# Performance work log

Measured on AMD Instinct MI355X. Metric: run time of the kernel, lower is better.

Reference implementation:

```python
import math
import jax, jax.numpy as jnp
import numpy as np

B, H, S, D = 1, 16, 4096, 64

def setup_inputs() -> dict:
    key = jax.random.key(0)
    kq, kk, kv = jax.random.split(key, 3)
    query = jax.random.normal(kq, (B, H, S, D), dtype=jnp.float32)
    k = jax.random.normal(kk, (B, H, S, D), dtype=jnp.float32)
    value = jax.random.normal(kv, (B, H, S, D), dtype=jnp.float32)
    return {"query": query, "key": k, "value": value}

def reference(query, key, value):
    # scale_factor = 1/sqrt(head_dim) (scale arg defaults to None)
    scale = 1.0 / math.sqrt(query.shape[-1])
    # bmm1: [B,H,L,S] scores; invAttnHead applies the scale inside the hpu softmax,
    # equivalent to scaling scores before a standard softmax
    scores = jnp.einsum('bhld,bhsd->bhls', query, key) * scale
    attn = jax.nn.softmax(scores, axis=-1)
    # dropout_p defaults to 0.0 -> identity; attn_bias in the original is dead code
    return jnp.einsum('bhls,bhsd->bhld', attn, value)
```

## Files before the change

kernel.cpp:

```cpp
#include <hip/hip_runtime.h>


#define SQ 4096
#define DH 64
#define KVB 64
#define VSTRIDE 72

#define QSCALE 0.1803368801111204f

typedef __attribute__((ext_vector_type(8))) short short8;
typedef __attribute__((ext_vector_type(4))) short short4v;
typedef __attribute__((ext_vector_type(4))) float f32x4;

static __device__ __forceinline__ short f2b(float f) {
  __bf16 h = (__bf16)f;
  return (short)__builtin_bit_cast(unsigned short, h);
}

static __device__ __forceinline__ float exp2_fast(float x) {
  return __builtin_amdgcn_exp2f(x);
}

#define MFMA16(a, b, c) __builtin_amdgcn_mfma_f32_16x16x32_bf16((a), (b), (c), 0, 0, 0)

__global__ __launch_bounds__(256, 2) void attn_fwd(const float* __restrict__ Q,
                                                   const float* __restrict__ K,
                                                   const float* __restrict__ V,
                                                   float* __restrict__ O) {
  __shared__ unsigned short Klds[64 * 64];
  __shared__ unsigned short Vtlds[64 * VSTRIDE];
  __shared__ unsigned short Plds[4 * 32 * 64];

  const int bid = blockIdx.x;
  const int h = (bid & 7) + 8 * (bid >> 8);
  const int qtile = (bid >> 3) & 31;
  const int tid = threadIdx.x;
  const int w = tid >> 6;
  const int lane = tid & 63;
  const int g = lane >> 4;
  const int c16 = lane & 15;

  const float* Qh = Q + h * SQ * DH;
  const float* Kh = K + h * SQ * DH;
  const float* Vh = V + h * SQ * DH;
  float* Oh = O + h * SQ * DH;

  const int qbase = qtile * 128 + w * 32;

  const f32x4 zero4 = {0.f, 0.f, 0.f, 0.f};

  short8 qb[2][2];
#pragma unroll
  for (int qt = 0; qt < 2; ++qt) {
    const float* qr = Qh + (qbase + qt * 16 + c16) * DH + 8 * g;
#pragma unroll
    for (int c = 0; c < 2; ++c) {
      float4 a = *(const float4*)(qr + 32 * c);
      float4 b = *(const float4*)(qr + 32 * c + 4);
      short8 f;
      f[0] = f2b(a.x * QSCALE); f[1] = f2b(a.y * QSCALE);
      f[2] = f2b(a.z * QSCALE); f[3] = f2b(a.w * QSCALE);
      f[4] = f2b(b.x * QSCALE); f[5] = f2b(b.y * QSCALE);
      f[6] = f2b(b.z * QSCALE); f[7] = f2b(b.w * QSCALE);
      qb[qt][c] = f;
    }
  }

  f32x4 Oacc[2][4];
#pragma unroll
  for (int qt = 0; qt < 2; ++qt)
#pragma unroll
    for (int dt = 0; dt < 4; ++dt) Oacc[qt][dt] = zero4;
  float mrun[2] = {-INFINITY, -INFINITY};
  float lrun[2] = {0.f, 0.f};

  const int sk = 4 * (tid >> 4);
  const int sd = 4 * (tid & 15);

  for (int t = 0; t < SQ / KVB; ++t) {
    const int kv0 = t * KVB;
    __syncthreads();

    {
      const float* kb = Kh + (kv0 + sk) * DH + sd;
      const float* vb = Vh + (kv0 + sk) * DH + sd;
      float4 k0 = *(const float4*)(kb + 0 * DH);
      float4 k1 = *(const float4*)(kb + 1 * DH);
      float4 k2 = *(const float4*)(kb + 2 * DH);
      float4 k3 = *(const float4*)(kb + 3 * DH);
      float4 v0 = *(const float4*)(vb + 0 * DH);
      float4 v1 = *(const float4*)(vb + 1 * DH);
      float4 v2 = *(const float4*)(vb + 2 * DH);
      float4 v3 = *(const float4*)(vb + 3 * DH);

      short4v a;
      a[0] = f2b(k0.x); a[1] = f2b(k0.y); a[2] = f2b(k0.z); a[3] = f2b(k0.w);
      *(short4v*)&Klds[(sk + 0) * 64 + (sd ^ (((sk + 0) & 7) * 8))] = a;
      a[0] = f2b(k1.x); a[1] = f2b(k1.y); a[2] = f2b(k1.z); a[3] = f2b(k1.w);
      *(short4v*)&Klds[(sk + 1) * 64 + (sd ^ (((sk + 1) & 7) * 8))] = a;
      a[0] = f2b(k2.x); a[1] = f2b(k2.y); a[2] = f2b(k2.z); a[3] = f2b(k2.w);
      *(short4v*)&Klds[(sk + 2) * 64 + (sd ^ (((sk + 2) & 7) * 8))] = a;
      a[0] = f2b(k3.x); a[1] = f2b(k3.y); a[2] = f2b(k3.z); a[3] = f2b(k3.w);
      *(short4v*)&Klds[(sk + 3) * 64 + (sd ^ (((sk + 3) & 7) * 8))] = a;

      short4v tv;
      tv[0] = f2b(v0.x); tv[1] = f2b(v1.x); tv[2] = f2b(v2.x); tv[3] = f2b(v3.x);
      *(short4v*)&Vtlds[(sd + 0) * VSTRIDE + sk] = tv;
      tv[0] = f2b(v0.y); tv[1] = f2b(v1.y); tv[2] = f2b(v2.y); tv[3] = f2b(v3.y);
      *(short4v*)&Vtlds[(sd + 1) * VSTRIDE + sk] = tv;
      tv[0] = f2b(v0.z); tv[1] = f2b(v1.z); tv[2] = f2b(v2.z); tv[3] = f2b(v3.z);
      *(short4v*)&Vtlds[(sd + 2) * VSTRIDE + sk] = tv;
      tv[0] = f2b(v0.w); tv[1] = f2b(v1.w); tv[2] = f2b(v2.w); tv[3] = f2b(v3.w);
      *(short4v*)&Vtlds[(sd + 3) * VSTRIDE + sk] = tv;
    }
    __syncthreads();

    f32x4 sA[2][4];
#pragma unroll
    for (int kt = 0; kt < 4; ++kt) {
      const int roff = (kt * 16 + c16) * 64;
      const int sw = (c16 & 7) * 8;
      short8 ka0 = *(const short8*)&Klds[roff + ((8 * g) ^ sw)];
      short8 ka1 = *(const short8*)&Klds[roff + ((8 * g + 32) ^ sw)];
      sA[0][kt] = MFMA16(ka0, qb[0][0], zero4);
      sA[0][kt] = MFMA16(ka1, qb[0][1], sA[0][kt]);
      sA[1][kt] = MFMA16(ka0, qb[1][0], zero4);
      sA[1][kt] = MFMA16(ka1, qb[1][1], sA[1][kt]);
    }

#pragma unroll
    for (int qt = 0; qt < 2; ++qt) {
      float mx = sA[qt][0][0];
#pragma unroll
      for (int kt = 0; kt < 4; ++kt)
#pragma unroll
        for (int r = 0; r < 4; ++r) mx = fmaxf(mx, sA[qt][kt][r]);
      mx = fmaxf(mx, __shfl_xor(mx, 16));
      mx = fmaxf(mx, __shfl_xor(mx, 32));
      const float mnew = fmaxf(mrun[qt], mx);
      const float fsc = exp2_fast(mrun[qt] - mnew);
      mrun[qt] = mnew;

      float psum = 0.f;
      const int prow = (w * 32 + qt * 16 + c16) * 64;
      const int psw = (c16 & 7) * 8;
#pragma unroll
      for (int kt = 0; kt < 4; ++kt) {
        float p0 = exp2_fast(sA[qt][kt][0] - mnew);
        float p1 = exp2_fast(sA[qt][kt][1] - mnew);
        float p2 = exp2_fast(sA[qt][kt][2] - mnew);
        float p3 = exp2_fast(sA[qt][kt][3] - mnew);
        psum += (p0 + p1) + (p2 + p3);
        short4v pw;
        pw[0] = f2b(p0); pw[1] = f2b(p1); pw[2] = f2b(p2); pw[3] = f2b(p3);
        *(short4v*)&Plds[prow + ((4 * g + 16 * kt) ^ psw)] = pw;
      }
      psum += __shfl_xor(psum, 16);
      psum += __shfl_xor(psum, 32);
      lrun[qt] = lrun[qt] * fsc + psum;

      const float f0 = __shfl(fsc, 4 * g + 0);
      const float f1 = __shfl(fsc, 4 * g + 1);
      const float f2 = __shfl(fsc, 4 * g + 2);
      const float f3 = __shfl(fsc, 4 * g + 3);
#pragma unroll
      for (int dt = 0; dt < 4; ++dt) {
        Oacc[qt][dt][0] *= f0;
        Oacc[qt][dt][1] *= f1;
        Oacc[qt][dt][2] *= f2;
        Oacc[qt][dt][3] *= f3;
      }
    }

#pragma unroll
    for (int c = 0; c < 2; ++c) {
      const int koff = (8 * g + 32 * c) ^ ((c16 & 7) * 8);
      short8 pa0 = *(const short8*)&Plds[(w * 32 + c16) * 64 + koff];
      short8 pa1 = *(const short8*)&Plds[(w * 32 + 16 + c16) * 64 + koff];
#pragma unroll
      for (int dt = 0; dt < 4; ++dt) {
        const int vroff = (dt * 16 + c16) * VSTRIDE + 8 * g + 32 * c;
        short4v lo = *(const short4v*)&Vtlds[vroff];
        short4v hi = *(const short4v*)&Vtlds[vroff + 4];
        short8 vbf;
        vbf[0] = lo[0]; vbf[1] = lo[1]; vbf[2] = lo[2]; vbf[3] = lo[3];
        vbf[4] = hi[0]; vbf[5] = hi[1]; vbf[6] = hi[2]; vbf[7] = hi[3];
        Oacc[0][dt] = MFMA16(pa0, vbf, Oacc[0][dt]);
        Oacc[1][dt] = MFMA16(pa1, vbf, Oacc[1][dt]);
      }
    }
  }

#pragma unroll
  for (int qt = 0; qt < 2; ++qt) {
    const float inv = 1.0f / lrun[qt];
    const float i0 = __shfl(inv, 4 * g + 0);
    const float i1 = __shfl(inv, 4 * g + 1);
    const float i2 = __shfl(inv, 4 * g + 2);
    const float i3 = __shfl(inv, 4 * g + 3);
#pragma unroll
    for (int dt = 0; dt < 4; ++dt) {
      float* op = Oh + (qbase + qt * 16 + 4 * g) * DH + dt * 16 + c16;
      op[0 * DH] = Oacc[qt][dt][0] * i0;
      op[1 * DH] = Oacc[qt][dt][1] * i1;
      op[2 * DH] = Oacc[qt][dt][2] * i2;
      op[3 * DH] = Oacc[qt][dt][3] * i3;
    }
  }
}

extern "C" void kernel_launch(void* const* d_in, const int* in_sizes, int n_in,
                              void* d_out, int out_size, void* d_ws, size_t ws_size,
                              hipStream_t stream) {
  const float* q = (const float*)d_in[0];
  const float* k = (const float*)d_in[1];
  const float* v = (const float*)d_in[2];
  float* o = (float*)d_out;
  attn_fwd<<<dim3(512), dim3(256), 0, stream>>>(q, k, v, o);
}
```

Measured before the change: 226.2 us.

## Double-buffer K/V tiles, use 8 waves of 16 rows, skip redundant rescale

Doubles the block to 512 threads so each wave owns 16 query rows instead of 32. K/V tiles are double-buffered in LDS, with the next tile's global loads issued before the current tile's compute, which removes one barrier per iteration. Output rescaling is skipped when the wave-wide max does not grow, and s_setprio raises priority around the MFMA sections. The trade-off is more LDS, more waves per block, and K/V staging spread over twice as many threads, each of which converts less data.

```diff
diff --git a/kernel.cpp b/kernel.cpp
--- a/kernel.cpp
+++ b/kernel.cpp
@@ -4,12 +4,14 @@
 #define SQ 4096
 #define DH 64
 #define KVB 64
+#define NT (SQ / KVB)
 #define VSTRIDE 72
 
 #define QSCALE 0.1803368801111204f
 
 typedef __attribute__((ext_vector_type(8))) short short8;
 typedef __attribute__((ext_vector_type(4))) short short4v;
+typedef __attribute__((ext_vector_type(2))) short short2v;
 typedef __attribute__((ext_vector_type(4))) float f32x4;
 
 static __device__ __forceinline__ short f2b(float f) {
@@ -23,13 +25,13 @@
 
 #define MFMA16(a, b, c) __builtin_amdgcn_mfma_f32_16x16x32_bf16((a), (b), (c), 0, 0, 0)
 
-__global__ __launch_bounds__(256, 2) void attn_fwd(const float* __restrict__ Q,
+__global__ __launch_bounds__(512, 4) void attn_fwd(const float* __restrict__ Q,
                                                    const float* __restrict__ K,
                                                    const float* __restrict__ V,
                                                    float* __restrict__ O) {
-  __shared__ unsigned short Klds[64 * 64];
-  __shared__ unsigned short Vtlds[64 * VSTRIDE];
-  __shared__ unsigned short Plds[4 * 32 * 64];
+  __shared__ unsigned short Klds[2][64 * 64];
+  __shared__ unsigned short Vtlds[2][64 * VSTRIDE];
+  __shared__ unsigned short Plds[8 * 16 * 64];
 
   const int bid = blockIdx.x;
   const int h = (bid & 7) + 8 * (bid >> 8);
@@ -45,14 +47,13 @@
   const float* Vh = V + h * SQ * DH;
   float* Oh = O + h * SQ * DH;
 
-  const int qbase = qtile * 128 + w * 32;
+  const int qbase = qtile * 128 + w * 16;
 
   const f32x4 zero4 = {0.f, 0.f, 0.f, 0.f};
 
-  short8 qb[2][2];
-#pragma unroll
-  for (int qt = 0; qt < 2; ++qt) {
-    const float* qr = Qh + (qbase + qt * 16 + c16) * DH + 8 * g;
+  short8 qb[2];
+  {
+    const float* qr = Qh + (qbase + c16) * DH + 8 * g;
 #pragma unroll
     for (int c = 0; c < 2; ++c) {
       float4 a = *(const float4*)(qr + 32 * c);
@@ -62,94 +63,110 @@
       f[2] = f2b(a.z * QSCALE); f[3] = f2b(a.w * QSCALE);
       f[4] = f2b(b.x * QSCALE); f[5] = f2b(b.y * QSCALE);
       f[6] = f2b(b.z * QSCALE); f[7] = f2b(b.w * QSCALE);
-      qb[qt][c] = f;
-    }
-  }
-
-  f32x4 Oacc[2][4];
-#pragma unroll
-  for (int qt = 0; qt < 2; ++qt)
-#pragma unroll
-    for (int dt = 0; dt < 4; ++dt) Oacc[qt][dt] = zero4;
-  float mrun[2] = {-INFINITY, -INFINITY};
-  float lrun[2] = {0.f, 0.f};
-
-  const int sk = 4 * (tid >> 4);
+      qb[c] = f;
+    }
+  }
+
+  f32x4 Oacc[4];
+#pragma unroll
+  for (int dt = 0; dt < 4; ++dt) Oacc[dt] = zero4;
+  float mrun = -INFINITY;
+  float lrun = 0.f;
+
+  const int sk = 2 * (tid >> 4);
   const int sd = 4 * (tid & 15);
-
-  for (int t = 0; t < SQ / KVB; ++t) {
-    const int kv0 = t * KVB;
+  const int skv = 2 * (tid & 31);
+  const int sdv = 4 * (tid >> 5);
+
+  float4 k0, k1, v0, v1;
+#define LOAD_TILE(kv0)                                  \
+  {                                                     \
+    const float* kb = Kh + ((kv0) + sk) * DH + sd;      \
+    const float* vb = Vh + ((kv0) + skv) * DH + sdv;    \
+    k0 = *(const float4*)(kb + 0 * DH);                 \
+    k1 = *(const float4*)(kb + 1 * DH);                 \
+    v0 = *(const float4*)(vb + 0 * DH);                 \
+    v1 = *(const float4*)(vb + 1 * DH);                 \
+  }
+
+#define WRITE_TILE(b)                                                       \
+  {                                                                         \
+    short4v a;                                                              \
+    a[0] = f2b(k0.x); a[1] = f2b(k0.y); a[2] = f2b(k0.z); a[3] = f2b(k0.w); \
+    *(short4v*)&Klds[b][(sk + 0) * 64 + (sd ^ (((sk + 0) & 7) * 8))] = a;   \
+    a[0] = f2b(k1.x); a[1] = f2b(k1.y); a[2] = f2b(k1.z); a[3] = f2b(k1.w); \
+    *(short4v*)&Klds[b][(sk + 1) * 64 + (sd ^ (((sk + 1) & 7) * 8))] = a;   \
+    short2v tv;                                                             \
+    tv[0] = f2b(v0.x); tv[1] = f2b(v1.x);                                   \
+    *(short2v*)&Vtlds[b][(sdv + 0) * VSTRIDE + skv] = tv;                   \
+    tv[0] = f2b(v0.y); tv[1] = f2b(v1.y);                                   \
+    *(short2v*)&Vtlds[b][(sdv + 1) * VSTRIDE + skv] = tv;                   \
+    tv[0] = f2b(v0.z); tv[1] = f2b(v1.z);                                   \
+    *(short2v*)&Vtlds[b][(sdv + 2) * VSTRIDE + skv] = tv;                   \
+    tv[0] = f2b(v0.w); tv[1] = f2b(v1.w);                                   \
+    *(short2v*)&Vtlds[b][(sdv + 3) * VSTRIDE + skv] = tv;                   \
+  }
+
+  LOAD_TILE(0)
+  WRITE_TILE(0)
+  int cur = 0;
+
+  for (int t = 0; t < NT; ++t) {
     __syncthreads();
 
-    {
-      const float* kb = Kh + (kv0 + sk) * DH + sd;
-      const float* vb = Vh + (kv0 + sk) * DH + sd;
-      float4 k0 = *(const float4*)(kb + 0 * DH);
-      float4 k1 = *(const float4*)(kb + 1 * DH);
-      float4 k2 = *(const float4*)(kb + 2 * DH);
-      float4 k3 = *(const float4*)(kb + 3 * DH);
-      float4 v0 = *(const float4*)(vb + 0 * DH);
-      float4 v1 = *(const float4*)(vb + 1 * DH);
-      float4 v2 = *(const float4*)(vb + 2 * DH);
-      float4 v3 = *(const float4*)(vb + 3 * DH);
-
-      short4v a;
-      a[0] = f2b(k0.x); a[1] = f2b(k0.y); a[2] = f2b(k0.z); a[3] = f2b(k0.w);
-      *(short4v*)&Klds[(sk + 0) * 64 + (sd ^ (((sk + 0) & 7) * 8))] = a;
-      a[0] = f2b(k1.x); a[1] = f2b(k1.y); a[2] = f2b(k1.z); a[3] = f2b(k1.w);
-      *(short4v*)&Klds[(sk + 1) * 64 + (sd ^ (((sk + 1) & 7) * 8))] = a;
-      a[0] = f2b(k2.x); a[1] = f2b(k2.y); a[2] = f2b(k2.z); a[3] = f2b(k2.w);
-      *(short4v*)&Klds[(sk + 2) * 64 + (sd ^ (((sk + 2) & 7) * 8))] = a;
-      a[0] = f2b(k3.x); a[1] = f2b(k3.y); a[2] = f2b(k3.z); a[3] = f2b(k3.w);
-      *(short4v*)&Klds[(sk + 3) * 64 + (sd ^ (((sk + 3) & 7) * 8))] = a;
-
-      short4v tv;
-      tv[0] = f2b(v0.x); tv[1] = f2b(v1.x); tv[2] = f2b(v2.x); tv[3] = f2b(v3.x);
-      *(short4v*)&Vtlds[(sd + 0) * VSTRIDE + sk] = tv;
-      tv[0] = f2b(v0.y); tv[1] = f2b(v1.y); tv[2] = f2b(v2.y); tv[3] = f2b(v3.y);
-      *(short4v*)&Vtlds[(sd + 1) * VSTRIDE + sk] = tv;
-      tv[0] = f2b(v0.z); tv[1] = f2b(v1.z); tv[2] = f2b(v2.z); tv[3] = f2b(v3.z);
-      *(short4v*)&Vtlds[(sd + 2) * VSTRIDE + sk] = tv;
-      tv[0] = f2b(v0.w); tv[1] = f2b(v1.w); tv[2] = f2b(v2.w); tv[3] = f2b(v3.w);
-      *(short4v*)&Vtlds[(sd + 3) * VSTRIDE + sk] = tv;
-    }
-    __syncthreads();
-
-    f32x4 sA[2][4];
+    const int tn = (t + 1 < NT) ? (t + 1) : t;
+    LOAD_TILE(tn * KVB)
+
+    f32x4 sA[4];
+    __builtin_amdgcn_s_setprio(1);
 #pragma unroll
     for (int kt = 0; kt < 4; ++kt) {
       const int roff = (kt * 16 + c16) * 64;
       const int sw = (c16 & 7) * 8;
-      short8 ka0 = *(const short8*)&Klds[roff + ((8 * g) ^ sw)];
-      short8 ka1 = *(const short8*)&Klds[roff + ((8 * g + 32) ^ sw)];
-      sA[0][kt] = MFMA16(ka0, qb[0][0], zero4);
-      sA[0][kt] = MFMA16(ka1, qb[0][1], sA[0][kt]);
-      sA[1][kt] = MFMA16(ka0, qb[1][0], zero4);
-      sA[1][kt] = MFMA16(ka1, qb[1][1], sA[1][kt]);
-    }
-
-#pragma unroll
-    for (int qt = 0; qt < 2; ++qt) {
-      float mx = sA[qt][0][0];
+      short8 ka0 = *(const short8*)&Klds[cur][roff + ((8 * g) ^ sw)];
+      short8 ka1 = *(const short8*)&Klds[cur][roff + ((8 * g + 32) ^ sw)];
+      sA[kt] = MFMA16(ka0, qb[0], zero4);
+      sA[kt] = MFMA16(ka1, qb[1], sA[kt]);
+    }
+    __builtin_amdgcn_s_setprio(0);
+
+    {
+      float mx = sA[0][0];
 #pragma unroll
       for (int kt = 0; kt < 4; ++kt)
 #pragma unroll
-        for (int r = 0; r < 4; ++r) mx = fmaxf(mx, sA[qt][kt][r]);
+        for (int r = 0; r < 4; ++r) mx = fmaxf(mx, sA[kt][r]);
       mx = fmaxf(mx, __shfl_xor(mx, 16));
       mx = fmaxf(mx, __shfl_xor(mx, 32));
-      const float mnew = fmaxf(mrun[qt], mx);
-      const float fsc = exp2_fast(mrun[qt] - mnew);
-      mrun[qt] = mnew;
-
+
+      if (!__all(mx <= mrun)) {
+        const float mnew = fmaxf(mrun, mx);
+        const float fsc = exp2_fast(mrun - mnew);
+        mrun = mnew;
+        lrun *= fsc;
+        const float f0 = __shfl(fsc, 4 * g + 0);
+        const float f1 = __shfl(fsc, 4 * g + 1);
+        const float f2 = __shfl(fsc, 4 * g + 2);
+        const float f3 = __shfl(fsc, 4 * g + 3);
+#pragma unroll
+        for (int dt = 0; dt < 4; ++dt) {
+          Oacc[dt][0] *= f0;
+          Oacc[dt][1] *= f1;
+          Oacc[dt][2] *= f2;
+          Oacc[dt][3] *= f3;
+        }
+      }
+
+      const float mcur = mrun;
       float psum = 0.f;
-      const int prow = (w * 32 + qt * 16 + c16) * 64;
+      const int prow = (w * 16 + c16) * 64;
       const int psw = (c16 & 7) * 8;
 #pragma unroll
       for (int kt = 0; kt < 4; ++kt) {
-        float p0 = exp2_fast(sA[qt][kt][0] - mnew);
-        float p1 = exp2_fast(sA[qt][kt][1] - mnew);
-        float p2 = exp2_fast(sA[qt][kt][2] - mnew);
-        float p3 = exp2_fast(sA[qt][kt][3] - mnew);
+        float p0 = exp2_fast(sA[kt][0] - mcur);
+        float p1 = exp2_fast(sA[kt][1] - mcur);
+        float p2 = exp2_fast(sA[kt][2] - mcur);
+        float p3 = exp2_fast(sA[kt][3] - mcur);
         psum += (p0 + p1) + (p2 + p3);
         short4v pw;
         pw[0] = f2b(p0); pw[1] = f2b(p1); pw[2] = f2b(p2); pw[3] = f2b(p3);
@@ -157,54 +174,44 @@
       }
       psum += __shfl_xor(psum, 16);
       psum += __shfl_xor(psum, 32);
-      lrun[qt] = lrun[qt] * fsc + psum;
-
-      const float f0 = __shfl(fsc, 4 * g + 0);
-      const float f1 = __shfl(fsc, 4 * g + 1);
-      const float f2 = __shfl(fsc, 4 * g + 2);
-      const float f3 = __shfl(fsc, 4 * g + 3);
-#pragma unroll
-      for (int dt = 0; dt < 4; ++dt) {
-        Oacc[qt][dt][0] *= f0;
-        Oacc[qt][dt][1] *= f1;
-        Oacc[qt][dt][2] *= f2;
-        Oacc[qt][dt][3] *= f3;
-      }
-    }
-
+      lrun += psum;
+    }
+
+    __builtin_amdgcn_s_setprio(1);
 #pragma unroll
     for (int c = 0; c < 2; ++c) {
       const int koff = (8 * g + 32 * c) ^ ((c16 & 7) * 8);
-      short8 pa0 = *(const short8*)&Plds[(w * 32 + c16) * 64 + koff];
-      short8 pa1 = *(const short8*)&Plds[(w * 32 + 16 + c16) * 64 + koff];
+      short8 pa = *(const short8*)&Plds[(w * 16 + c16) * 64 + koff];
 #pragma unroll
       for (int dt = 0; dt < 4; ++dt) {
         const int vroff = (dt * 16 + c16) * VSTRIDE + 8 * g + 32 * c;
-        short4v lo = *(const short4v*)&Vtlds[vroff];
-        short4v hi = *(const short4v*)&Vtlds[vroff + 4];
+        short4v lo = *(const short4v*)&Vtlds[cur][vroff];
+        short4v hi = *(const short4v*)&Vtlds[cur][vroff + 4];
         short8 vbf;
         vbf[0] = lo[0]; vbf[1] = lo[1]; vbf[2] = lo[2]; vbf[3] = lo[3];
         vbf[4] = hi[0]; vbf[5] = hi[1]; vbf[6] = hi[2]; vbf[7] = hi[3];
-        Oacc[0][dt] = MFMA16(pa0, vbf, Oacc[0][dt]);
-        Oacc[1][dt] = MFMA16(pa1, vbf, Oacc[1][dt]);
+        Oacc[dt] = MFMA16(pa, vbf, Oacc[dt]);
       }
     }
-  }
-
-#pragma unroll
-  for (int qt = 0; qt < 2; ++qt) {
-    const float inv = 1.0f / lrun[qt];
+    __builtin_amdgcn_s_setprio(0);
+
+    WRITE_TILE(cur ^ 1)
+    cur ^= 1;
+  }
+
+  {
+    const float inv = 1.0f / lrun;
     const float i0 = __shfl(inv, 4 * g + 0);
     const float i1 = __shfl(inv, 4 * g + 1);
     const float i2 = __shfl(inv, 4 * g + 2);
     const float i3 = __shfl(inv, 4 * g + 3);
 #pragma unroll
     for (int dt = 0; dt < 4; ++dt) {
-      float* op = Oh + (qbase + qt * 16 + 4 * g) * DH + dt * 16 + c16;
-      op[0 * DH] = Oacc[qt][dt][0] * i0;
-      op[1 * DH] = Oacc[qt][dt][1] * i1;
-      op[2 * DH] = Oacc[qt][dt][2] * i2;
-      op[3 * DH] = Oacc[qt][dt][3] * i3;
+      float* op = Oh + (qbase + 4 * g) * DH + dt * 16 + c16;
+      op[0 * DH] = Oacc[dt][0] * i0;
+      op[1 * DH] = Oacc[dt][1] * i1;
+      op[2 * DH] = Oacc[dt][2] * i2;
+      op[3 * DH] = Oacc[dt][3] * i3;
     }
   }
 }
@@ -216,5 +223,5 @@
   const float* k = (const float*)d_in[1];
   const float* v = (const float*)d_in[2];
   float* o = (float*)d_out;
-  attn_fwd<<<dim3(512), dim3(256), 0, stream>>>(q, k, v, o);
-}
+  attn_fwd<<<dim3(512), dim3(512), 0, stream>>>(q, k, v, o);
+}
```

Result: faster. 195.8 us (-13.4%).
